# Optimization experiments

Measured on AMD Instinct MI355X. Metric: run time of the kernel, lower is better.

Reference implementation:

```python
import jax, jax.numpy as jnp
import numpy as np

DIM = 128
NHEADS = 8
N = 4096
ALPHA = 0.2  # LeakyReLU negative slope
EPS = 1e-5   # LayerNorm eps


def setup_inputs() -> dict:
    key = jax.random.key(0)
    ks = jax.random.split(key, 8)
    s = 1.0 / np.sqrt(DIM)
    nodes = jax.random.normal(ks[0], (N, DIM), dtype=jnp.float32)
    adj = jax.random.randint(ks[1], (N, N), 0, 2, dtype=jnp.int32)
    # per-head GAT params: W [H,D,D], attention vectors a1,a2 [H,D]
    W = jax.random.normal(ks[2], (NHEADS, DIM, DIM), dtype=jnp.float32) * s
    a1 = jax.random.normal(ks[3], (NHEADS, DIM), dtype=jnp.float32) * s
    a2 = jax.random.normal(ks[4], (NHEADS, DIM), dtype=jnp.float32) * s
    # linear1: (dim*nheads) -> dim
    W1 = jax.random.normal(ks[5], (NHEADS * DIM, DIM), dtype=jnp.float32) * (1.0 / np.sqrt(NHEADS * DIM))
    b1 = jnp.zeros((DIM,), dtype=jnp.float32)
    gamma = jnp.ones((DIM,), dtype=jnp.float32)
    beta = jnp.zeros((DIM,), dtype=jnp.float32)
    return {"nodes": nodes, "adj": adj, "W": W, "a1": a1, "a2": a2,
            "W1": W1, "b1": b1, "gamma": gamma, "beta": beta}


def _layernorm(x, gamma, beta):
    mu = jnp.mean(x, axis=-1, keepdims=True)
    var = jnp.mean((x - mu) ** 2, axis=-1, keepdims=True)
    return (x - mu) * jax.lax.rsqrt(var + EPS) * gamma + beta


def reference(nodes, adj, W, a1, a2, W1, b1, gamma, beta):
    # Eval mode: all dropouts are identity.
    # Multi-head GAT: Wh [H, N, D]
    Wh = jnp.einsum('nd,hde->hne', nodes, W)
    f1 = jnp.einsum('hnd,hd->hn', Wh, a1)   # [H, N]
    f2 = jnp.einsum('hnd,hd->hn', Wh, a2)   # [H, N]
    e = jax.nn.leaky_relu(f1[:, :, None] + f2[:, None, :], negative_slope=ALPHA)  # [H,N,N]
    mask = (adj > 0)[None, :, :]
    att = jnp.where(mask, e, jnp.float32(-9e15))
    att = jax.nn.softmax(att, axis=-1)
    h = jnp.einsum('hnm,hmd->hnd', att, Wh)  # [H, N, D]
    h = jax.nn.elu(h)
    # concat heads along feature dim -> [N, H*D]
    cat = jnp.transpose(h, (1, 0, 2)).reshape(N, NHEADS * DIM)
    x = jax.nn.elu(cat @ W1 + b1)            # [N, D]
    out = _layernorm(nodes + x, gamma, beta)
    return out
```

## Files before the change

kernel.cpp:

```cpp
#include <hip/hip_runtime.h>
#include <hip/hip_bf16.h>


#define NN 4096
#define ALPHA 0.2f
#define EPSLN 1e-5f
#define LOG2E 1.4426950408889634f

typedef __attribute__((ext_vector_type(8))) _Float16 f16x8;
typedef __attribute__((ext_vector_type(4))) _Float16 f16x4;
typedef __attribute__((ext_vector_type(2))) _Float16 f16x2;
typedef __attribute__((ext_vector_type(4))) float f32x4;
typedef __attribute__((ext_vector_type(4))) int i32x4;

union F16x8 { f16x8 v; f16x2 h[4]; };
union F16x4 { f16x4 v; f16x2 h[2]; };

static __device__ inline f16x2 pkrtz(float a, float b) {
  union { decltype(__builtin_amdgcn_cvt_pkrtz(0.f, 0.f)) r; f16x2 h; } u;
  u.r = __builtin_amdgcn_cvt_pkrtz(a, b);
  return u.h;
}

#if __has_builtin(__builtin_amdgcn_exp2f)
#define EXP2(x) __builtin_amdgcn_exp2f(x)
#else
#define EXP2(x) exp2f(x)
#endif

static __device__ __forceinline__ void gload16(const void* g, void* l) {
  __builtin_amdgcn_global_load_lds(
      (const __attribute__((address_space(1))) void*)g,
      (__attribute__((address_space(3))) void*)l, 16, 0, 0);
}

static __device__ inline unsigned long long sp4(unsigned long long x) {
  x = (x | (x << 24)) & 0x000000FF000000FFULL;
  x = (x | (x << 12)) & 0x000F000F000F000FULL;
  x = (x | (x << 6))  & 0x0303030303030303ULL;
  x = (x | (x << 3))  & 0x1111111111111111ULL;
  return x;
}

__global__ void k_packprep(const int* __restrict__ adj, unsigned long long* __restrict__ maskT,
                           const float* __restrict__ W, const float* __restrict__ W1,
                           _Float16* __restrict__ Wt, _Float16* __restrict__ W1t) {
  int bid = blockIdx.x;
  if (bid < 16384) {
    int wv = threadIdx.x >> 6, l = threadIdx.x & 63;
    int gid = bid * 4 + wv;
    int row = gid >> 4, chunk = gid & 15;
    i32x4 v = *(const i32x4*)(adj + ((size_t)row << 12) + chunk * 256 + l * 4);
    unsigned long long b0 = __ballot(v.x > 0);
    unsigned long long b1 = __ballot(v.y > 0);
    unsigned long long b2 = __ballot(v.z > 0);
    unsigned long long b3 = __ballot(v.w > 0);
    if (l < 4) {
      int sh = l * 16;
      unsigned long long w = sp4((b0 >> sh) & 0xFFFF)
                           | (sp4((b1 >> sh) & 0xFFFF) << 1)
                           | (sp4((b2 >> sh) & 0xFFFF) << 2)
                           | (sp4((b3 >> sh) & 0xFFFF) << 3);
      maskT[(size_t)(chunk * 4 + l) * NN + row] = w;
    }
  } else {
    int idx = (bid - 16384) * 256 + threadIdx.x;
    if (idx < 131072) {
      int h = idx >> 14, r = idx & 16383, d = r >> 7, e = r & 127;
      Wt[h * 16384 + e * 128 + d] = (_Float16)W[idx];
    } else {
      int j = idx - 131072;
      int k = j >> 7, d = j & 127;
      W1t[d * 1024 + k] = (_Float16)W1[j];
    }
  }
}

__global__ __launch_bounds__(256) void k_wh(const float* __restrict__ nodes,
    const _Float16* __restrict__ Wt, const float* __restrict__ a1,
    const float* __restrict__ a2, _Float16* __restrict__ Whbt,
    float* __restrict__ f1L, float* __restrict__ f2L) {
  int h = blockIdx.y;
  int wv = threadIdx.x >> 6, l = threadIdx.x & 63;
  int lr = l & 15, lg = l >> 4;
  int ibase = blockIdx.x * 64 + wv * 16;
  f32x4 acc[8] = {};
  const float* arow = nodes + (size_t)(ibase + lr) * 128;
  const _Float16* bbase = Wt + h * 16384;
#pragma unroll
  for (int ks = 0; ks < 4; ++ks) {
    int k0 = ks * 32 + lg * 8;
    f32x4 av0 = *(const f32x4*)(arow + k0);
    f32x4 av1 = *(const f32x4*)(arow + k0 + 4);
    F16x8 A;
    A.h[0] = pkrtz(av0[0], av0[1]);
    A.h[1] = pkrtz(av0[2], av0[3]);
    A.h[2] = pkrtz(av1[0], av1[1]);
    A.h[3] = pkrtz(av1[2], av1[3]);
#pragma unroll
    for (int nt = 0; nt < 8; ++nt) {
      f16x8 B = *(const f16x8*)(bbase + (nt * 16 + lr) * 128 + k0);
      acc[nt] = __builtin_amdgcn_mfma_f32_16x16x32_f16(A.v, B, acc[nt], 0, 0, 0);
    }
  }
#pragma unroll
  for (int nt = 0; nt < 8; ++nt) {
    F16x4 o;
    o.h[0] = pkrtz(acc[nt][0], acc[nt][1]);
    o.h[1] = pkrtz(acc[nt][2], acc[nt][3]);
    *(f16x4*)(Whbt + (size_t)(h * 128 + nt * 16 + lr) * NN + ibase + lg * 4) = o.v;
  }
  float a1r[8], a2r[8];
#pragma unroll
  for (int nt = 0; nt < 8; ++nt) {
    a1r[nt] = a1[h * 128 + nt * 16 + lr];
    a2r[nt] = a2[h * 128 + nt * 16 + lr];
  }
#pragma unroll
  for (int r = 0; r < 4; ++r) {
    float s1 = 0.f, s2 = 0.f;
#pragma unroll
    for (int nt = 0; nt < 8; ++nt) { s1 += acc[nt][r] * a1r[nt]; s2 += acc[nt][r] * a2r[nt]; }
    s1 += __shfl_xor(s1, 1, 16); s1 += __shfl_xor(s1, 2, 16);
    s1 += __shfl_xor(s1, 4, 16); s1 += __shfl_xor(s1, 8, 16);
    s2 += __shfl_xor(s2, 1, 16); s2 += __shfl_xor(s2, 2, 16);
    s2 += __shfl_xor(s2, 4, 16); s2 += __shfl_xor(s2, 8, 16);
    if (lr == 0) {
      int i = ibase + lg * 4 + r;
      f1L[h * NN + i] = s1 * LOG2E;
      f2L[h * NN + i] = s2 * LOG2E;
    }
  }
}

__global__ __launch_bounds__(1024) void k_m2(const float* __restrict__ f2L,
    float* __restrict__ M2L, float2* __restrict__ e2t) {
  __shared__ float red[16];
  int h = blockIdx.x, t = threadIdx.x;
  float a[4];
#pragma unroll
  for (int i = 0; i < 4; ++i) a[i] = f2L[h * NN + t + i * 1024];
  float v = fmaxf(fmaxf(a[0], a[1]), fmaxf(a[2], a[3]));
#pragma unroll
  for (int off = 1; off < 64; off <<= 1) v = fmaxf(v, __shfl_xor(v, off, 64));
  if ((t & 63) == 0) red[t >> 6] = v;
  __syncthreads();
  if (t < 16) {
    float m = red[t];
#pragma unroll
    for (int off = 1; off < 16; off <<= 1) m = fmaxf(m, __shfl_xor(m, off, 16));
    if (t == 0) { red[0] = m; M2L[h] = m; }
  }
  __syncthreads();
  float M2 = red[0];
#pragma unroll
  for (int i = 0; i < 4; ++i) {
    float d = a[i] - M2;
    float2 e; e.x = EXP2(d); e.y = EXP2(ALPHA * d);
    e2t[h * NN + t + i * 1024] = e;
  }
}

__global__ __launch_bounds__(256, 2) void k_attn(const _Float16* __restrict__ Whbt,
    const float* __restrict__ f1L, const float* __restrict__ M2L,
    const float2* __restrict__ e2t, const unsigned long long* __restrict__ maskT,
    _Float16* __restrict__ hcat) {
  __shared__ __align__(16) char Bt[2][32768];
  __shared__ float denL[64];
  int t = threadIdx.x, w = t >> 6, l = t & 63, lr = l & 15, lg = l >> 4;
  int bid = blockIdx.x;
  int h = bid & 7;
  int rowbase = (bid >> 3) * 64;
  int rh = w >> 1, jh = w & 1;
  int r0 = rowbase + rh * 32 + lr, r1 = r0 + 16;
  float f10 = f1L[h * NN + r0], f11 = f1L[h * NN + r1];
  float M2 = M2L[h];
  float s0 = f10 + M2, s1 = f11 + M2;
  float mL0 = fmaxf(s0, ALPHA * s0), mL1 = fmaxf(s1, ALPHA * s1);
  float E10 = EXP2(s0 - mL0), Ea0 = EXP2(ALPHA * s0 - mL0);
  float E11 = EXP2(s1 - mL1), Ea1 = EXP2(ALPHA * s1 - mL1);
  f32x4 acc0[8] = {}, acc1[8] = {};
  float den0 = 0.f, den1 = 0.f;
  const _Float16* src = Whbt + ((size_t)h << 19);
  const float* ep = (const float*)(e2t + (size_t)h * NN);

  int t4 = t >> 4;
  int jc = (t & 15) ^ (t4 & 15);
  size_t goff = (size_t)t4 * NN + jc * 8;

  {
    const _Float16* gp = src + goff;
    char* lb = &Bt[0][0] + t * 16;
#pragma unroll
    for (int p = 0; p < 8; ++p)
      gload16(gp + (size_t)p * 16 * NN, lb + p * 4096);
  }
  __syncthreads();

  for (int ct = 0; ct < 32; ++ct) {
    if (ct + 1 < 32) {
      const _Float16* gp = src + goff + (ct + 1) * 128;
      char* lb = &Bt[(ct + 1) & 1][0] + t * 16;
#pragma unroll
      for (int p = 0; p < 8; ++p)
        gload16(gp + (size_t)p * 16 * NN, lb + p * 4096);
    }
    unsigned long long m0 = maskT[(size_t)(ct * 2 + jh) * NN + r0];
    unsigned long long m1 = maskT[(size_t)(ct * 2 + jh) * NN + r1];
    const char* btr = &Bt[ct & 1][0];
    const float* eq = ep + (ct * 128 + jh * 64) * 2;
#pragma unroll
    for (int ks = 0; ks < 2; ++ks) {
      const float* e2p = eq + (ks * 32 + lg * 8) * 2;
      f32x4 Q[4];
#pragma unroll
      for (int c = 0; c < 4; ++c) Q[c] = *(const f32x4*)(e2p + c * 4);
      int sh = ks * 32 + lg * 8;
      unsigned bits0 = (unsigned)(m0 >> sh);
      unsigned bits1 = (unsigned)(m1 >> sh);
      float p0[8], p1[8];
#pragma unroll
      for (int e = 0; e < 8; ++e) {
        float e2 = Q[e >> 1][(e & 1) * 2];
        float e2a = Q[e >> 1][(e & 1) * 2 + 1];
        float v0 = fmaxf(E10 * e2, Ea0 * e2a);
        p0[e] = ((bits0 >> e) & 1) ? v0 : 0.f;
        den0 += p0[e];
        float v1 = fmaxf(E11 * e2, Ea1 * e2a);
        p1[e] = ((bits1 >> e) & 1) ? v1 : 0.f;
        den1 += p1[e];
      }
      F16x8 A0, A1;
#pragma unroll
      for (int qq = 0; qq < 4; ++qq) {
        A0.h[qq] = pkrtz(p0[2 * qq], p0[2 * qq + 1]);
        A1.h[qq] = pkrtz(p1[2 * qq], p1[2 * qq + 1]);
      }
      int slotbase = jh * 8 + ks * 4 + lg;
#pragma unroll
      for (int nt = 0; nt < 8; ++nt) {
        int d = nt * 16 + lr;
        int byteoff = d * 256 + ((slotbase ^ lr) << 4);
        f16x8 B = *(const f16x8*)(btr + byteoff);
        acc0[nt] = __builtin_amdgcn_mfma_f32_16x16x32_f16(A0.v, B, acc0[nt], 0, 0, 0);
        acc1[nt] = __builtin_amdgcn_mfma_f32_16x16x32_f16(A1.v, B, acc1[nt], 0, 0, 0);
      }
    }
    __syncthreads();
  }
  den0 += __shfl_xor(den0, 16, 64); den0 += __shfl_xor(den0, 32, 64);
  den1 += __shfl_xor(den1, 16, 64); den1 += __shfl_xor(den1, 32, 64);

  float* reg = (float*)Bt + (size_t)rh * 32 * 132;
  if (jh == 0) {
#pragma unroll
    for (int nt = 0; nt < 8; ++nt)
#pragma unroll
      for (int r = 0; r < 4; ++r) {
        reg[(lg * 4 + r) * 132 + nt * 16 + lr] = acc0[nt][r];
        reg[(16 + lg * 4 + r) * 132 + nt * 16 + lr] = acc1[nt][r];
      }
    if (l < 16) { denL[rh * 32 + lr] = den0; denL[rh * 32 + 16 + lr] = den1; }
  }
  __syncthreads();
  if (jh == 1) {
#pragma unroll
    for (int nt = 0; nt < 8; ++nt)
#pragma unroll
      for (int r = 0; r < 4; ++r) {
        reg[(lg * 4 + r) * 132 + nt * 16 + lr] += acc0[nt][r];
        reg[(16 + lg * 4 + r) * 132 + nt * 16 + lr] += acc1[nt][r];
      }
    if (l < 16) { denL[rh * 32 + lr] += den0; denL[rh * 32 + 16 + lr] += den1; }
  }
  __syncthreads();
  {
    int row = t >> 2, seg = t & 3;
    const float* rg = (float*)Bt + (size_t)(row >> 5) * 32 * 132 + (row & 31) * 132 + seg * 32;
    float rc = __builtin_amdgcn_rcpf(denL[row]);
    _Float16* outp = hcat + (size_t)(rowbase + row) * 1024 + h * 128 + seg * 32;
#pragma unroll
    for (int q8 = 0; q8 < 4; ++q8) {
      f32x4 va = *(const f32x4*)(rg + q8 * 8);
      f32x4 vb = *(const f32x4*)(rg + q8 * 8 + 4);
      float x[8];
#pragma unroll
      for (int c = 0; c < 4; ++c) { x[c] = va[c] * rc; x[4 + c] = vb[c] * rc; }
#pragma unroll
      for (int c = 0; c < 8; ++c) x[c] = x[c] > 0.f ? x[c] : EXP2(x[c] * LOG2E) - 1.f;
      F16x8 o;
      o.h[0] = pkrtz(x[0], x[1]); o.h[1] = pkrtz(x[2], x[3]);
      o.h[2] = pkrtz(x[4], x[5]); o.h[3] = pkrtz(x[6], x[7]);
      *(f16x8*)(outp + q8 * 8) = o.v;
    }
  }
}

__global__ __launch_bounds__(256) void k_out(const _Float16* __restrict__ hcat,
    const _Float16* __restrict__ W1t, const float* __restrict__ b1,
    const float* __restrict__ nodes, const float* __restrict__ gamma,
    const float* __restrict__ beta, float* __restrict__ out) {
  __shared__ __align__(16) float part[4][16][132];
  int t = threadIdx.x, w = t >> 6, l = t & 63, lr = l & 15, lg = l >> 4;
  int ibase = blockIdx.x * 16;
  f32x4 acc[8] = {};
  const _Float16* arow = hcat + (size_t)(ibase + lr) * 1024 + w * 256;
  const _Float16* bb = W1t + w * 256;
#pragma unroll
  for (int ks = 0; ks < 8; ++ks) {
    int k0 = ks * 32 + lg * 8;
    f16x8 A = *(const f16x8*)(arow + k0);
#pragma unroll
    for (int nt = 0; nt < 8; ++nt) {
      f16x8 B = *(const f16x8*)(bb + (nt * 16 + lr) * 1024 + k0);
      acc[nt] = __builtin_amdgcn_mfma_f32_16x16x32_f16(A, B, acc[nt], 0, 0, 0);
    }
  }
#pragma unroll
  for (int nt = 0; nt < 8; ++nt)
#pragma unroll
    for (int r = 0; r < 4; ++r)
      part[w][lg * 4 + r][nt * 16 + lr] = acc[nt][r];
  __syncthreads();
  int row = t >> 4, c16 = t & 15;
  int d0 = c16 * 8;
  size_t gi = (size_t)(ibase + row) * 128;
  f32x4 pa = {}, pb = {};
#pragma unroll
  for (int q = 0; q < 4; ++q) {
    pa += *(const f32x4*)&part[q][row][d0];
    pb += *(const f32x4*)&part[q][row][d0 + 4];
  }
  f32x4 ba = *(const f32x4*)(b1 + d0), bbv = *(const f32x4*)(b1 + d0 + 4);
  f32x4 na = *(const f32x4*)(nodes + gi + d0), nb = *(const f32x4*)(nodes + gi + d0 + 4);
  float y[8];
  float sum = 0.f, sq = 0.f;
#pragma unroll
  for (int c = 0; c < 4; ++c) {
    float x = pa[c] + ba[c];
    x = x > 0.f ? x : EXP2(x * LOG2E) - 1.f;
    y[c] = x + na[c];
    float x2 = pb[c] + bbv[c];
    x2 = x2 > 0.f ? x2 : EXP2(x2 * LOG2E) - 1.f;
    y[4 + c] = x2 + nb[c];
  }
#pragma unroll
  for (int c = 0; c < 8; ++c) { sum += y[c]; sq += y[c] * y[c]; }
#pragma unroll
  for (int off = 1; off < 16; off <<= 1) {
    sum += __shfl_xor(sum, off, 16);
    sq += __shfl_xor(sq, off, 16);
  }
  float mu = sum * (1.f / 128.f);
  float var = sq * (1.f / 128.f) - mu * mu;
  float rs = __builtin_amdgcn_rsqf(var + EPSLN);
  f32x4 ga = *(const f32x4*)(gamma + d0), gb = *(const f32x4*)(gamma + d0 + 4);
  f32x4 bea = *(const f32x4*)(beta + d0), beb = *(const f32x4*)(beta + d0 + 4);
  f32x4 o0, o1;
#pragma unroll
  for (int c = 0; c < 4; ++c) {
    o0[c] = (y[c] - mu) * rs * ga[c] + bea[c];
    o1[c] = (y[4 + c] - mu) * rs * gb[c] + beb[c];
  }
  *(f32x4*)(out + gi + d0) = o0;
  *(f32x4*)(out + gi + d0 + 4) = o1;
}

extern "C" void kernel_launch(void* const* d_in, const int* in_sizes, int n_in,
                              void* d_out, int out_size, void* d_ws, size_t ws_size,
                              hipStream_t stream) {
  const float* nodes = (const float*)d_in[0];
  const int* adj = (const int*)d_in[1];
  const float* W = (const float*)d_in[2];
  const float* a1 = (const float*)d_in[3];
  const float* a2 = (const float*)d_in[4];
  const float* W1 = (const float*)d_in[5];
  const float* b1 = (const float*)d_in[6];
  const float* gamma = (const float*)d_in[7];
  const float* beta = (const float*)d_in[8];
  float* out = (float*)d_out;
  char* ws = (char*)d_ws;

  const size_t OFF_MASK = 0;
  const size_t OFF_WHBT = 2097152;
  const size_t OFF_F1 = OFF_WHBT + 8388608;
  const size_t OFF_F2 = OFF_F1 + 131072;
  const size_t OFF_M2 = OFF_F2 + 131072;
  const size_t OFF_E2T = OFF_M2 + 256;
  const size_t OFF_WT = OFF_E2T + 262144;
  const size_t OFF_W1T = OFF_WT + 262144;
  const size_t OFF_HCAT = OFF_W1T + 262144;

  unsigned long long* maskT = (unsigned long long*)(ws + OFF_MASK);
  _Float16* Whbt = (_Float16*)(ws + OFF_WHBT);
  float* f1L = (float*)(ws + OFF_F1);
  float* f2L = (float*)(ws + OFF_F2);
  float* M2L = (float*)(ws + OFF_M2);
  float2* e2t = (float2*)(ws + OFF_E2T);
  _Float16* Wt = (_Float16*)(ws + OFF_WT);
  _Float16* W1t = (_Float16*)(ws + OFF_W1T);
  _Float16* hcat = (_Float16*)(ws + OFF_HCAT);

  k_packprep<<<17408, 256, 0, stream>>>(adj, maskT, W, W1, Wt, W1t);
  k_wh<<<dim3(64, 8), 256, 0, stream>>>(nodes, Wt, a1, a2, Whbt, f1L, f2L);
  k_m2<<<8, 1024, 0, stream>>>(f2L, M2L, e2t);
  k_attn<<<512, 256, 0, stream>>>(Whbt, f1L, M2L, e2t, maskT, hcat);
  k_out<<<256, 256, 0, stream>>>(hcat, W1t, b1, nodes, gamma, beta, out);
}
```

Before: 104.1 us.

## Shrink attention tile, compute probabilities in packed fp16, stage e2 in LDS

The attention kernel now gives each block 32 rows instead of 64, with one 16-row MMA set per wave. The grid doubles to 1024 blocks and launch bounds allow 4 blocks per CU, using 16KB LDS buffers and 64-column chunks. The softmax numerators are computed in packed fp16 with bitmask masking and an fdot2 reduction for the denominator. The e2 factors are stored as fp16 planes and staged into LDS with async loads. The mask load is prefetched one step ahead and s_setprio is raised around the MFMA burst. The trade is higher occupancy and less VALU work against half the reuse of each Wh tile, twice the Wh traffic per row, and lower-precision exponent products.

New measurement: 118.2 us. +13.6%, slower.

```diff
diff --git a/kernel.cpp b/kernel.cpp
--- a/kernel.cpp
+++ b/kernel.cpp
@@ -12,9 +12,11 @@
 typedef __attribute__((ext_vector_type(2))) _Float16 f16x2;
 typedef __attribute__((ext_vector_type(4))) float f32x4;
 typedef __attribute__((ext_vector_type(4))) int i32x4;
+typedef __fp16 h16x2 __attribute__((ext_vector_type(2)));
 
 union F16x8 { f16x8 v; f16x2 h[4]; };
 union F16x4 { f16x4 v; f16x2 h[2]; };
+union PKU { f16x2 f; unsigned u; };
 
 static __device__ inline f16x2 pkrtz(float a, float b) {
   union { decltype(__builtin_amdgcn_cvt_pkrtz(0.f, 0.f)) r; f16x2 h; } u;
@@ -27,6 +29,16 @@
 #else
 #define EXP2(x) exp2f(x)
 #endif
+
+static __device__ __forceinline__ float fdot2f(f16x2 a, f16x2 b, float c) {
+#if __has_builtin(__builtin_amdgcn_fdot2)
+  union { f16x2 f; h16x2 h; } ua, ub;
+  ua.f = a; ub.f = b;
+  return __builtin_amdgcn_fdot2(ua.h, ub.h, c, false);
+#else
+  return c + (float)a[0] * (float)b[0] + (float)a[1] * (float)b[1];
+#endif
+}
 
 static __device__ __forceinline__ void gload16(const void* g, void* l) {
   __builtin_amdgcn_global_load_lds(
@@ -134,7 +146,7 @@
 }
 
 __global__ __launch_bounds__(1024) void k_m2(const float* __restrict__ f2L,
-    float* __restrict__ M2L, float2* __restrict__ e2t) {
+    float* __restrict__ M2L, _Float16* __restrict__ e2ph) {
   __shared__ float red[16];
   int h = blockIdx.x, t = threadIdx.x;
   float a[4];
@@ -156,131 +168,123 @@
 #pragma unroll
   for (int i = 0; i < 4; ++i) {
     float d = a[i] - M2;
-    float2 e; e.x = EXP2(d); e.y = EXP2(ALPHA * d);
-    e2t[h * NN + t + i * 1024] = e;
-  }
-}
-
-__global__ __launch_bounds__(256, 2) void k_attn(const _Float16* __restrict__ Whbt,
+    e2ph[h * 8192 + t + i * 1024] = (_Float16)EXP2(d);
+    e2ph[h * 8192 + 4096 + t + i * 1024] = (_Float16)EXP2(ALPHA * d);
+  }
+}
+
+__global__ __launch_bounds__(256, 4) void k_attn(const _Float16* __restrict__ Whbt,
     const float* __restrict__ f1L, const float* __restrict__ M2L,
-    const float2* __restrict__ e2t, const unsigned long long* __restrict__ maskT,
+    const _Float16* __restrict__ e2ph, const unsigned long long* __restrict__ maskT,
     _Float16* __restrict__ hcat) {
-  __shared__ __align__(16) char Bt[2][32768];
-  __shared__ float denL[64];
+  __shared__ __align__(16) char Bt[2][16384];
+  __shared__ __align__(16) _Float16 e2s[2][128];
+  __shared__ float denL[32];
   int t = threadIdx.x, w = t >> 6, l = t & 63, lr = l & 15, lg = l >> 4;
   int bid = blockIdx.x;
   int h = bid & 7;
-  int rowbase = (bid >> 3) * 64;
+  int rowbase = (bid >> 3) * 32;
   int rh = w >> 1, jh = w & 1;
-  int r0 = rowbase + rh * 32 + lr, r1 = r0 + 16;
-  float f10 = f1L[h * NN + r0], f11 = f1L[h * NN + r1];
+  int r0 = rowbase + rh * 16 + lr;
+  float f10 = f1L[h * NN + r0];
   float M2 = M2L[h];
-  float s0 = f10 + M2, s1 = f11 + M2;
-  float mL0 = fmaxf(s0, ALPHA * s0), mL1 = fmaxf(s1, ALPHA * s1);
-  float E10 = EXP2(s0 - mL0), Ea0 = EXP2(ALPHA * s0 - mL0);
-  float E11 = EXP2(s1 - mL1), Ea1 = EXP2(ALPHA * s1 - mL1);
-  f32x4 acc0[8] = {}, acc1[8] = {};
-  float den0 = 0.f, den1 = 0.f;
+  float s0 = f10 + M2;
+  float mL0 = fmaxf(s0, ALPHA * s0);
+  f16x2 E1pk = pkrtz(EXP2(s0 - mL0), EXP2(s0 - mL0));
+  f16x2 Eapk = pkrtz(EXP2(ALPHA * s0 - mL0), EXP2(ALPHA * s0 - mL0));
+  f16x2 ones = pkrtz(1.f, 1.f);
+  f32x4 acc[8] = {};
+  float den = 0.f;
   const _Float16* src = Whbt + ((size_t)h << 19);
-  const float* ep = (const float*)(e2t + (size_t)h * NN);
-
-  int t4 = t >> 4;
-  int jc = (t & 15) ^ (t4 & 15);
-  size_t goff = (size_t)t4 * NN + jc * 8;
+  const _Float16* ept = e2ph + h * 8192;
+
+  int jc = (t & 7) ^ ((t >> 3) & 7);
+  size_t gA = ((size_t)(t >> 3) << 12) + jc * 8;
+  size_t gE = (size_t)(((t >> 3) & 1) * 4096) + (t & 7) * 8;
 
   {
-    const _Float16* gp = src + goff;
+    const _Float16* gp = src + gA;
     char* lb = &Bt[0][0] + t * 16;
 #pragma unroll
-    for (int p = 0; p < 8; ++p)
-      gload16(gp + (size_t)p * 16 * NN, lb + p * 4096);
-  }
-  __syncthreads();
-
-  for (int ct = 0; ct < 32; ++ct) {
-    if (ct + 1 < 32) {
-      const _Float16* gp = src + goff + (ct + 1) * 128;
+    for (int p = 0; p < 4; ++p)
+      gload16(gp + (size_t)p * 131072, lb + p * 4096);
+    if (t < 16) gload16(ept + gE, (char*)&e2s[0][0] + t * 16);
+  }
+  unsigned long long m = maskT[r0];
+  __syncthreads();
+
+  for (int ct = 0; ct < 64; ++ct) {
+    unsigned long long mn = 0;
+    if (ct + 1 < 64) {
+      mn = maskT[(size_t)(ct + 1) * NN + r0];
+      const _Float16* gp = src + gA + (ct + 1) * 64;
       char* lb = &Bt[(ct + 1) & 1][0] + t * 16;
 #pragma unroll
-      for (int p = 0; p < 8; ++p)
-        gload16(gp + (size_t)p * 16 * NN, lb + p * 4096);
-    }
-    unsigned long long m0 = maskT[(size_t)(ct * 2 + jh) * NN + r0];
-    unsigned long long m1 = maskT[(size_t)(ct * 2 + jh) * NN + r1];
+      for (int p = 0; p < 4; ++p)
+        gload16(gp + (size_t)p * 131072, lb + p * 4096);
+      if (t < 16) gload16(ept + gE + (ct + 1) * 64, (char*)&e2s[(ct + 1) & 1][0] + t * 16);
+    }
     const char* btr = &Bt[ct & 1][0];
-    const float* eq = ep + (ct * 128 + jh * 64) * 2;
-#pragma unroll
-    for (int ks = 0; ks < 2; ++ks) {
-      const float* e2p = eq + (ks * 32 + lg * 8) * 2;
-      f32x4 Q[4];
-#pragma unroll
-      for (int c = 0; c < 4; ++c) Q[c] = *(const f32x4*)(e2p + c * 4);
-      int sh = ks * 32 + lg * 8;
-      unsigned bits0 = (unsigned)(m0 >> sh);
-      unsigned bits1 = (unsigned)(m1 >> sh);
-      float p0[8], p1[8];
-#pragma unroll
-      for (int e = 0; e < 8; ++e) {
-        float e2 = Q[e >> 1][(e & 1) * 2];
-        float e2a = Q[e >> 1][(e & 1) * 2 + 1];
-        float v0 = fmaxf(E10 * e2, Ea0 * e2a);
-        p0[e] = ((bits0 >> e) & 1) ? v0 : 0.f;
-        den0 += p0[e];
-        float v1 = fmaxf(E11 * e2, Ea1 * e2a);
-        p1[e] = ((bits1 >> e) & 1) ? v1 : 0.f;
-        den1 += p1[e];
-      }
-      F16x8 A0, A1;
-#pragma unroll
-      for (int qq = 0; qq < 4; ++qq) {
-        A0.h[qq] = pkrtz(p0[2 * qq], p0[2 * qq + 1]);
-        A1.h[qq] = pkrtz(p1[2 * qq], p1[2 * qq + 1]);
-      }
-      int slotbase = jh * 8 + ks * 4 + lg;
-#pragma unroll
-      for (int nt = 0; nt < 8; ++nt) {
-        int d = nt * 16 + lr;
-        int byteoff = d * 256 + ((slotbase ^ lr) << 4);
-        f16x8 B = *(const f16x8*)(btr + byteoff);
-        acc0[nt] = __builtin_amdgcn_mfma_f32_16x16x32_f16(A0.v, B, acc0[nt], 0, 0, 0);
-        acc1[nt] = __builtin_amdgcn_mfma_f32_16x16x32_f16(A1.v, B, acc1[nt], 0, 0, 0);
-      }
-    }
+    const _Float16* e2p = &e2s[ct & 1][0];
+    unsigned bits = (unsigned)(m >> (jh * 32 + lg * 8)) & 0xFFu;
+    F16x8 e2u = *(const F16x8*)(e2p + jh * 32 + lg * 8);
+    F16x8 e2au = *(const F16x8*)(e2p + 64 + jh * 32 + lg * 8);
+    F16x8 A;
+#pragma unroll
+    for (int pi = 0; pi < 4; ++pi) {
+      f16x2 t1 = E1pk * e2u.h[pi];
+      f16x2 t2 = Eapk * e2au.h[pi];
+      f16x2 mx;
+      mx[0] = t1[0] > t2[0] ? t1[0] : t2[0];
+      mx[1] = t1[1] > t2[1] ? t1[1] : t2[1];
+      unsigned b = (bits >> (2 * pi)) & 3u;
+      unsigned msk = ((b & 1u) ? 0xFFFFu : 0u) | ((b & 2u) ? 0xFFFF0000u : 0u);
+      PKU um; um.f = mx; um.u &= msk;
+      A.h[pi] = um.f;
+      den = fdot2f(um.f, ones, den);
+    }
+    __builtin_amdgcn_s_setprio(1);
+#pragma unroll
+    for (int nt = 0; nt < 8; ++nt) {
+      int d = nt * 16 + lr;
+      int byteoff = d * 128 + (((jh * 4 + lg) ^ (d & 7)) << 4);
+      f16x8 B = *(const f16x8*)(btr + byteoff);
+      acc[nt] = __builtin_amdgcn_mfma_f32_16x16x32_f16(A.v, B, acc[nt], 0, 0, 0);
+    }
+    __builtin_amdgcn_s_setprio(0);
     __syncthreads();
-  }
-  den0 += __shfl_xor(den0, 16, 64); den0 += __shfl_xor(den0, 32, 64);
-  den1 += __shfl_xor(den1, 16, 64); den1 += __shfl_xor(den1, 32, 64);
-
-  float* reg = (float*)Bt + (size_t)rh * 32 * 132;
+    m = mn;
+  }
+  den += __shfl_xor(den, 16, 64);
+  den += __shfl_xor(den, 32, 64);
+
+  float* cmb = (float*)Bt;
+  float* reg = cmb + (size_t)rh * 16 * 132;
   if (jh == 0) {
 #pragma unroll
     for (int nt = 0; nt < 8; ++nt)
 #pragma unroll
-      for (int r = 0; r < 4; ++r) {
-        reg[(lg * 4 + r) * 132 + nt * 16 + lr] = acc0[nt][r];
-        reg[(16 + lg * 4 + r) * 132 + nt * 16 + lr] = acc1[nt][r];
-      }
-    if (l < 16) { denL[rh * 32 + lr] = den0; denL[rh * 32 + 16 + lr] = den1; }
+      for (int r = 0; r < 4; ++r)
+        reg[(lg * 4 + r) * 132 + nt * 16 + lr] = acc[nt][r];
+    if (l < 16) denL[rh * 16 + lr] = den;
   }
   __syncthreads();
   if (jh == 1) {
 #pragma unroll
     for (int nt = 0; nt < 8; ++nt)
 #pragma unroll
-      for (int r = 0; r < 4; ++r) {
-        reg[(lg * 4 + r) * 132 + nt * 16 + lr] += acc0[nt][r];
-        reg[(16 + lg * 4 + r) * 132 + nt * 16 + lr] += acc1[nt][r];
-      }
-    if (l < 16) { denL[rh * 32 + lr] += den0; denL[rh * 32 + 16 + lr] += den1; }
+      for (int r = 0; r < 4; ++r)
+        reg[(lg * 4 + r) * 132 + nt * 16 + lr] += acc[nt][r];
+    if (l < 16) denL[rh * 16 + lr] += den;
   }
   __syncthreads();
   {
-    int row = t >> 2, seg = t & 3;
-    const float* rg = (float*)Bt + (size_t)(row >> 5) * 32 * 132 + (row & 31) * 132 + seg * 32;
+    int row = t >> 3, seg = t & 7;
+    const float* rg = cmb + (size_t)(row >> 4) * 16 * 132 + (row & 15) * 132 + seg * 16;
     float rc = __builtin_amdgcn_rcpf(denL[row]);
-    _Float16* outp = hcat + (size_t)(rowbase + row) * 1024 + h * 128 + seg * 32;
-#pragma unroll
-    for (int q8 = 0; q8 < 4; ++q8) {
+    _Float16* outp = hcat + (size_t)(rowbase + row) * 1024 + h * 128 + seg * 16;
+#pragma unroll
+    for (int q8 = 0; q8 < 2; ++q8) {
       f32x4 va = *(const f32x4*)(rg + q8 * 8);
       f32x4 vb = *(const f32x4*)(rg + q8 * 8 + 4);
       float x[8];
@@ -387,7 +391,7 @@
   const size_t OFF_F2 = OFF_F1 + 131072;
   const size_t OFF_M2 = OFF_F2 + 131072;
   const size_t OFF_E2T = OFF_M2 + 256;
-  const size_t OFF_WT = OFF_E2T + 262144;
+  const size_t OFF_WT = OFF_E2T + 131072;
   const size_t OFF_W1T = OFF_WT + 262144;
   const size_t OFF_HCAT = OFF_W1T + 262144;
 
@@ -396,14 +400,14 @@
   float* f1L = (float*)(ws + OFF_F1);
   float* f2L = (float*)(ws + OFF_F2);
   float* M2L = (float*)(ws + OFF_M2);
-  float2* e2t = (float2*)(ws + OFF_E2T);
+  _Float16* e2ph = (_Float16*)(ws + OFF_E2T);
   _Float16* Wt = (_Float16*)(ws + OFF_WT);
   _Float16* W1t = (_Float16*)(ws + OFF_W1T);
   _Float16* hcat = (_Float16*)(ws + OFF_HCAT);
 
   k_packprep<<<17408, 256, 0, stream>>>(adj, maskT, W, W1, Wt, W1t);
   k_wh<<<dim3(64, 8), 256, 0, stream>>>(nodes, Wt, a1, a2, Whbt, f1L, f2L);
-  k_m2<<<8, 1024, 0, stream>>>(f2L, M2L, e2t);
-  k_attn<<<512, 256, 0, stream>>>(Whbt, f1L, M2L, e2t, maskT, hcat);
+  k_m2<<<8, 1024, 0, stream>>>(f2L, M2L, e2ph);
+  k_attn<<<1024, 256, 0, stream>>>(Whbt, f1L, M2L, e2ph, maskT, hcat);
   k_out<<<256, 256, 0, stream>>>(hcat, W1t, b1, nodes, gamma, beta, out);
 }
```

## Compute attention probabilities in packed fp16 and repartition waves over key columns

Applied to the files above, without the earlier changes.

The attention kernel now builds its softmax numerators with packed fp16 multiply and max instead of scalar fp32 math. The e2 factors are stored as separate fp16 planes and staged into shared memory through async global-to-LDS loads. Each wave now owns all 64 rows and a quarter of each 128-column tile, and the mask words are prefetched one tile ahead. The MFMA block is wrapped in s_setprio, and the partial accumulators of the four waves are combined in LDS in turn. This cuts VALU work and global traffic in the inner loop, but adds fp16 rounding to the probabilities and denominators, plus a serialized four-phase reduction.

Result: faster. 92.90 us (-10.7%).

```diff
diff --git a/kernel.cpp b/kernel.cpp
--- a/kernel.cpp
+++ b/kernel.cpp
@@ -12,9 +12,11 @@
 typedef __attribute__((ext_vector_type(2))) _Float16 f16x2;
 typedef __attribute__((ext_vector_type(4))) float f32x4;
 typedef __attribute__((ext_vector_type(4))) int i32x4;
-
-union F16x8 { f16x8 v; f16x2 h[4]; };
+typedef __fp16 h16x2 __attribute__((ext_vector_type(2)));
+
+union F16x8 { f16x8 v; f16x2 h[4]; unsigned u[4]; };
 union F16x4 { f16x4 v; f16x2 h[2]; };
+union PKU { f16x2 f; unsigned u; h16x2 r; };
 
 static __device__ inline f16x2 pkrtz(float a, float b) {
   union { decltype(__builtin_amdgcn_cvt_pkrtz(0.f, 0.f)) r; f16x2 h; } u;
@@ -27,6 +29,27 @@
 #else
 #define EXP2(x) exp2f(x)
 #endif
+
+static __device__ __forceinline__ unsigned pk_mul(unsigned a, unsigned b) {
+  unsigned d;
+  asm("v_pk_mul_f16 %0, %1, %2" : "=v"(d) : "v"(a), "v"(b));
+  return d;
+}
+static __device__ __forceinline__ unsigned pk_max(unsigned a, unsigned b) {
+  unsigned d;
+  asm("v_pk_max_f16 %0, %1, %2" : "=v"(d) : "v"(a), "v"(b));
+  return d;
+}
+
+static __device__ __forceinline__ float fdot2u(unsigned a, unsigned b, float c) {
+#if __has_builtin(__builtin_amdgcn_fdot2)
+  PKU ua, ub; ua.u = a; ub.u = b;
+  return __builtin_amdgcn_fdot2(ua.r, ub.r, c, false);
+#else
+  PKU ua, ub; ua.u = a; ub.u = b;
+  return c + (float)ua.f[0] * (float)ub.f[0] + (float)ua.f[1] * (float)ub.f[1];
+#endif
+}
 
 static __device__ __forceinline__ void gload16(const void* g, void* l) {
   __builtin_amdgcn_global_load_lds(
@@ -134,7 +157,7 @@
 }
 
 __global__ __launch_bounds__(1024) void k_m2(const float* __restrict__ f2L,
-    float* __restrict__ M2L, float2* __restrict__ e2t) {
+    float* __restrict__ M2L, _Float16* __restrict__ e2ph) {
   __shared__ float red[16];
   int h = blockIdx.x, t = threadIdx.x;
   float a[4];
@@ -156,133 +179,152 @@
 #pragma unroll
   for (int i = 0; i < 4; ++i) {
     float d = a[i] - M2;
-    float2 e; e.x = EXP2(d); e.y = EXP2(ALPHA * d);
-    e2t[h * NN + t + i * 1024] = e;
+    e2ph[h * 8192 + t + i * 1024] = (_Float16)EXP2(d);
+    e2ph[h * 8192 + 4096 + t + i * 1024] = (_Float16)EXP2(ALPHA * d);
   }
 }
 
 __global__ __launch_bounds__(256, 2) void k_attn(const _Float16* __restrict__ Whbt,
     const float* __restrict__ f1L, const float* __restrict__ M2L,
-    const float2* __restrict__ e2t, const unsigned long long* __restrict__ maskT,
+    const _Float16* __restrict__ e2ph, const unsigned long long* __restrict__ maskT,
     _Float16* __restrict__ hcat) {
   __shared__ __align__(16) char Bt[2][32768];
-  __shared__ float denL[64];
-  int t = threadIdx.x, w = t >> 6, l = t & 63, lr = l & 15, lg = l >> 4;
+  __shared__ __align__(16) _Float16 e2s[2][256];
+  __shared__ float denL[4][64];
+  int t = threadIdx.x, jq = t >> 6, l = t & 63, lr = l & 15, lg = l >> 4;
   int bid = blockIdx.x;
   int h = bid & 7;
   int rowbase = (bid >> 3) * 64;
-  int rh = w >> 1, jh = w & 1;
-  int r0 = rowbase + rh * 32 + lr, r1 = r0 + 16;
-  float f10 = f1L[h * NN + r0], f11 = f1L[h * NN + r1];
   float M2 = M2L[h];
-  float s0 = f10 + M2, s1 = f11 + M2;
-  float mL0 = fmaxf(s0, ALPHA * s0), mL1 = fmaxf(s1, ALPHA * s1);
-  float E10 = EXP2(s0 - mL0), Ea0 = EXP2(ALPHA * s0 - mL0);
-  float E11 = EXP2(s1 - mL1), Ea1 = EXP2(ALPHA * s1 - mL1);
-  f32x4 acc0[8] = {}, acc1[8] = {};
-  float den0 = 0.f, den1 = 0.f;
+  unsigned E1u[4], Eau[4];
+  int rg[4];
+#pragma unroll
+  for (int g = 0; g < 4; ++g) {
+    rg[g] = rowbase + g * 16 + lr;
+    float f1 = f1L[h * NN + rg[g]];
+    float s = f1 + M2;
+    float mL = fmaxf(s, ALPHA * s);
+    float e1 = EXP2(s - mL), ea = EXP2(ALPHA * s - mL);
+    PKU p1; p1.f = pkrtz(e1, e1); E1u[g] = p1.u;
+    PKU p2; p2.f = pkrtz(ea, ea); Eau[g] = p2.u;
+  }
+  f32x4 acc[4][8] = {};
+  float den[4] = {};
   const _Float16* src = Whbt + ((size_t)h << 19);
-  const float* ep = (const float*)(e2t + (size_t)h * NN);
+  const _Float16* ept = e2ph + h * 8192;
 
   int t4 = t >> 4;
   int jc = (t & 15) ^ (t4 & 15);
   size_t goff = (size_t)t4 * NN + jc * 8;
-
+  size_t gE = (size_t)(((t >> 4) & 1) * 4096) + (t & 15) * 8;
+  int mshift = (jq & 1) * 32 + lg * 8;
+  int wbase = jq >> 1;
+
+  unsigned long long mc[4];
+#pragma unroll
+  for (int g = 0; g < 4; ++g) mc[g] = maskT[(size_t)wbase * NN + rg[g]];
   {
     const _Float16* gp = src + goff;
     char* lb = &Bt[0][0] + t * 16;
 #pragma unroll
     for (int p = 0; p < 8; ++p)
       gload16(gp + (size_t)p * 16 * NN, lb + p * 4096);
+    if (t < 32) gload16(ept + gE, (char*)&e2s[0][0] + t * 16);
   }
   __syncthreads();
 
   for (int ct = 0; ct < 32; ++ct) {
+    unsigned long long mn[4] = {};
     if (ct + 1 < 32) {
+#pragma unroll
+      for (int g = 0; g < 4; ++g)
+        mn[g] = maskT[(size_t)((ct + 1) * 2 + wbase) * NN + rg[g]];
       const _Float16* gp = src + goff + (ct + 1) * 128;
       char* lb = &Bt[(ct + 1) & 1][0] + t * 16;
 #pragma unroll
       for (int p = 0; p < 8; ++p)
         gload16(gp + (size_t)p * 16 * NN, lb + p * 4096);
-    }
-    unsigned long long m0 = maskT[(size_t)(ct * 2 + jh) * NN + r0];
-    unsigned long long m1 = maskT[(size_t)(ct * 2 + jh) * NN + r1];
+      if (t < 32) gload16(ept + gE + (ct + 1) * 128, (char*)&e2s[(ct + 1) & 1][0] + t * 16);
+    }
     const char* btr = &Bt[ct & 1][0];
-    const float* eq = ep + (ct * 128 + jh * 64) * 2;
-#pragma unroll
-    for (int ks = 0; ks < 2; ++ks) {
-      const float* e2p = eq + (ks * 32 + lg * 8) * 2;
-      f32x4 Q[4];
-#pragma unroll
-      for (int c = 0; c < 4; ++c) Q[c] = *(const f32x4*)(e2p + c * 4);
-      int sh = ks * 32 + lg * 8;
-      unsigned bits0 = (unsigned)(m0 >> sh);
-      unsigned bits1 = (unsigned)(m1 >> sh);
-      float p0[8], p1[8];
-#pragma unroll
-      for (int e = 0; e < 8; ++e) {
-        float e2 = Q[e >> 1][(e & 1) * 2];
-        float e2a = Q[e >> 1][(e & 1) * 2 + 1];
-        float v0 = fmaxf(E10 * e2, Ea0 * e2a);
-        p0[e] = ((bits0 >> e) & 1) ? v0 : 0.f;
-        den0 += p0[e];
-        float v1 = fmaxf(E11 * e2, Ea1 * e2a);
-        p1[e] = ((bits1 >> e) & 1) ? v1 : 0.f;
-        den1 += p1[e];
+    const char* e2p = (const char*)&e2s[ct & 1][0];
+    i32x4 e2w = *(const i32x4*)(e2p + jq * 64 + lg * 16);
+    i32x4 e2aw = *(const i32x4*)(e2p + 256 + jq * 64 + lg * 16);
+    F16x8 afr[4];
+#pragma unroll
+    for (int g = 0; g < 4; ++g) {
+      unsigned bits = (unsigned)(mc[g] >> mshift) & 0xFFu;
+      float dg = den[g];
+#pragma unroll
+      for (int pi = 0; pi < 4; ++pi) {
+        unsigned mx = pk_max(pk_mul(E1u[g], (unsigned)e2w[pi]),
+                             pk_mul(Eau[g], (unsigned)e2aw[pi]));
+        unsigned b = (bits >> (2 * pi)) & 3u;
+        mx &= ((b & 1u) ? 0x0000FFFFu : 0u) | ((b & 2u) ? 0xFFFF0000u : 0u);
+        afr[g].u[pi] = mx;
+        dg = fdot2u(mx, 0x3C003C00u, dg);
       }
-      F16x8 A0, A1;
-#pragma unroll
-      for (int qq = 0; qq < 4; ++qq) {
-        A0.h[qq] = pkrtz(p0[2 * qq], p0[2 * qq + 1]);
-        A1.h[qq] = pkrtz(p1[2 * qq], p1[2 * qq + 1]);
+      den[g] = dg;
+    }
+    __builtin_amdgcn_s_setprio(1);
+#pragma unroll
+    for (int nt = 0; nt < 8; ++nt) {
+      int d = nt * 16 + lr;
+      int byteoff = d * 256 + (((jq * 4 + lg) ^ lr) << 4);
+      f16x8 B = *(const f16x8*)(btr + byteoff);
+#pragma unroll
+      for (int g = 0; g < 4; ++g)
+        acc[g][nt] = __builtin_amdgcn_mfma_f32_16x16x32_f16(afr[g].v, B, acc[g][nt], 0, 0, 0);
+    }
+    __builtin_amdgcn_s_setprio(0);
+    __syncthreads();
+#pragma unroll
+    for (int g = 0; g < 4; ++g) mc[g] = mn[g];
+  }
+#pragma unroll
+  for (int g = 0; g < 4; ++g) {
+    den[g] += __shfl_xor(den[g], 16, 64);
+    den[g] += __shfl_xor(den[g], 32, 64);
+  }
+  if (l < 16) {
+#pragma unroll
+    for (int g = 0; g < 4; ++g) denL[jq][g * 16 + lr] = den[g];
+  }
+
+  float* cmb = (float*)Bt;
+#pragma unroll
+  for (int ph = 0; ph < 4; ++ph) {
+    if (jq == ph) {
+      if (ph == 0) {
+#pragma unroll
+        for (int g = 0; g < 4; ++g)
+#pragma unroll
+          for (int nt = 0; nt < 8; ++nt)
+#pragma unroll
+            for (int r = 0; r < 4; ++r)
+              cmb[(g * 16 + lg * 4 + r) * 132 + nt * 16 + lr] = acc[g][nt][r];
+      } else {
+#pragma unroll
+        for (int g = 0; g < 4; ++g)
+#pragma unroll
+          for (int nt = 0; nt < 8; ++nt)
+#pragma unroll
+            for (int r = 0; r < 4; ++r)
+              cmb[(g * 16 + lg * 4 + r) * 132 + nt * 16 + lr] += acc[g][nt][r];
       }
-      int slotbase = jh * 8 + ks * 4 + lg;
-#pragma unroll
-      for (int nt = 0; nt < 8; ++nt) {
-        int d = nt * 16 + lr;
-        int byteoff = d * 256 + ((slotbase ^ lr) << 4);
-        f16x8 B = *(const f16x8*)(btr + byteoff);
-        acc0[nt] = __builtin_amdgcn_mfma_f32_16x16x32_f16(A0.v, B, acc0[nt], 0, 0, 0);
-        acc1[nt] = __builtin_amdgcn_mfma_f32_16x16x32_f16(A1.v, B, acc1[nt], 0, 0, 0);
-      }
     }
     __syncthreads();
   }
-  den0 += __shfl_xor(den0, 16, 64); den0 += __shfl_xor(den0, 32, 64);
-  den1 += __shfl_xor(den1, 16, 64); den1 += __shfl_xor(den1, 32, 64);
-
-  float* reg = (float*)Bt + (size_t)rh * 32 * 132;
-  if (jh == 0) {
-#pragma unroll
-    for (int nt = 0; nt < 8; ++nt)
-#pragma unroll
-      for (int r = 0; r < 4; ++r) {
-        reg[(lg * 4 + r) * 132 + nt * 16 + lr] = acc0[nt][r];
-        reg[(16 + lg * 4 + r) * 132 + nt * 16 + lr] = acc1[nt][r];
-      }
-    if (l < 16) { denL[rh * 32 + lr] = den0; denL[rh * 32 + 16 + lr] = den1; }
-  }
-  __syncthreads();
-  if (jh == 1) {
-#pragma unroll
-    for (int nt = 0; nt < 8; ++nt)
-#pragma unroll
-      for (int r = 0; r < 4; ++r) {
-        reg[(lg * 4 + r) * 132 + nt * 16 + lr] += acc0[nt][r];
-        reg[(16 + lg * 4 + r) * 132 + nt * 16 + lr] += acc1[nt][r];
-      }
-    if (l < 16) { denL[rh * 32 + lr] += den0; denL[rh * 32 + 16 + lr] += den1; }
-  }
-  __syncthreads();
   {
     int row = t >> 2, seg = t & 3;
-    const float* rg = (float*)Bt + (size_t)(row >> 5) * 32 * 132 + (row & 31) * 132 + seg * 32;
-    float rc = __builtin_amdgcn_rcpf(denL[row]);
+    const float* rgp = cmb + row * 132 + seg * 32;
+    float dsum = denL[0][row] + denL[1][row] + denL[2][row] + denL[3][row];
+    float rc = __builtin_amdgcn_rcpf(dsum);
     _Float16* outp = hcat + (size_t)(rowbase + row) * 1024 + h * 128 + seg * 32;
 #pragma unroll
     for (int q8 = 0; q8 < 4; ++q8) {
-      f32x4 va = *(const f32x4*)(rg + q8 * 8);
-      f32x4 vb = *(const f32x4*)(rg + q8 * 8 + 4);
+      f32x4 va = *(const f32x4*)(rgp + q8 * 8);
+      f32x4 vb = *(const f32x4*)(rgp + q8 * 8 + 4);
       float x[8];
 #pragma unroll
       for (int c = 0; c < 4; ++c) { x[c] = va[c] * rc; x[4 + c] = vb[c] * rc; }
@@ -387,7 +429,7 @@
   const size_t OFF_F2 = OFF_F1 + 131072;
   const size_t OFF_M2 = OFF_F2 + 131072;
   const size_t OFF_E2T = OFF_M2 + 256;
-  const size_t OFF_WT = OFF_E2T + 262144;
+  const size_t OFF_WT = OFF_E2T + 131072;
   const size_t OFF_W1T = OFF_WT + 262144;
   const size_t OFF_HCAT = OFF_W1T + 262144;
 
@@ -396,14 +438,14 @@
   float* f1L = (float*)(ws + OFF_F1);
   float* f2L = (float*)(ws + OFF_F2);
   float* M2L = (float*)(ws + OFF_M2);
-  float2* e2t = (float2*)(ws + OFF_E2T);
+  _Float16* e2ph = (_Float16*)(ws + OFF_E2T);
   _Float16* Wt = (_Float16*)(ws + OFF_WT);
   _Float16* W1t = (_Float16*)(ws + OFF_W1T);
   _Float16* hcat = (_Float16*)(ws + OFF_HCAT);
 
   k_packprep<<<17408, 256, 0, stream>>>(adj, maskT, W, W1, Wt, W1t);
   k_wh<<<dim3(64, 8), 256, 0, stream>>>(nodes, Wt, a1, a2, Whbt, f1L, f2L);
-  k_m2<<<8, 1024, 0, stream>>>(f2L, M2L, e2t);
-  k_attn<<<512, 256, 0, stream>>>(Whbt, f1L, M2L, e2t, maskT, hcat);
+  k_m2<<<8, 1024, 0, stream>>>(f2L, M2L, e2ph);
+  k_attn<<<512, 256, 0, stream>>>(Whbt, f1L, M2L, e2ph, maskT, hcat);
   k_out<<<256, 256, 0, stream>>>(hcat, W1t, b1, nodes, gamma, beta, out);
 }
```
